# Kernel tuning notes

Measured on AMD Instinct MI355X. Metric: run time of the kernel, lower is better.

The kernel has to match this reference:

```python
import jax, jax.numpy as jnp
import numpy as np

PATCH = 16      # sqrt(n_patches=256)
ALPHA = 10.0
HEADS, DH = 2, 64


def _fourier(coords, Bm):
    # coords: (HW, 2), Bm: (n_features, 2) -> (HW, 2*n_features)
    proj = 2.0 * jnp.pi * coords @ Bm.T
    return jnp.concatenate([jnp.cos(proj), jnp.sin(proj)], axis=-1)


def _forward(coords_decoding, tokens, B_q, B_l0, B_l1,
             qW, qb, toqW, tokvW, tooW, toob,
             bwW0, bwb0, bwW1, bwb1,
             modW0, modb0, modW1, modb1,
             hvW0, hvb0, outW0, outb0, outW1, outb1):
    B = coords_decoding.shape[0]
    Hh, Ww = coords_decoding.shape[1], coords_decoding.shape[2]
    coords = coords_decoding.reshape(B, -1, coords_decoding.shape[-1])
    grid = coords[0]                      # (HW, 2); coords_modulation is None -> same grid
    HW = grid.shape[0]
    m = tokens.shape[1]

    # patch indices and spatial bias
    row = jnp.clip((grid[:, 0] * PATCH).astype(jnp.int32), 0, PATCH - 1)
    col = jnp.clip((grid[:, 1] * PATCH).astype(jnp.int32), 0, PATCH - 1)
    idx = row * PATCH + col               # (HW,)
    t = idx.astype(jnp.float32) / (PATCH * PATCH)
    pos = (jnp.arange(m, dtype=jnp.float32) + 0.5) / m
    rel = -ALPHA * jnp.abs(t[None, :] - pos[:, None]) ** 2   # (m, HW)
    bias = rel.T                          # (HW, m), broadcast over batch & heads

    # query features (shared across batch)
    xq = jax.nn.relu(_fourier(grid, B_q) @ qW + qb)           # (HW, hd)
    xq_b = jnp.broadcast_to(xq[None], (B, HW, xq.shape[-1]))

    # cross attention with spatial bias
    q = (xq_b @ toqW).reshape(B, HW, HEADS, DH).transpose(0, 2, 1, 3)   # (B,h,HW,Dh)
    kv = tokens @ tokvW                                                  # (B,m,2*inner)
    k, v = jnp.split(kv, 2, axis=-1)
    k = k.reshape(B, m, HEADS, DH).transpose(0, 2, 1, 3)                 # (B,h,m,Dh)
    v = v.reshape(B, m, HEADS, DH).transpose(0, 2, 1, 3)
    sim = jnp.einsum('bhqd,bhkd->bhqk', q, k) * (DH ** -0.5) + bias[None, None]
    attn = jax.nn.softmax(sim, axis=-1)
    o = jnp.einsum('bhqk,bhkd->bhqd', attn, v)
    o = o.transpose(0, 2, 1, 3).reshape(B, HW, HEADS * DH)
    mod = o @ tooW + toob                                                # (B,HW,hd)

    # per-band MLP stack (layer_num = 2)
    def band(Bl, bwW, bwb, mW, mb):
        h = jax.nn.relu(_fourier(grid, Bl) @ bwW + bwb)                  # (HW,hd)
        return jax.nn.relu(h[None] + mod @ mW + mb)                      # (B,HW,hd)

    m0 = band(B_l0, bwW0, bwb0, modW0, modb0)
    m1 = band(B_l1, bwW1, bwb1, modW1, modb1)
    hv0 = m0
    hv1 = jax.nn.relu((m1 + hv0) @ hvW0 + hvb0)
    out = (hv0 @ outW0 + outb0) + (hv1 @ outW1 + outb1)                  # (B,HW,3)
    return out.reshape(B, Hh, Ww, -1)


def setup_inputs() -> dict:
    key = jax.random.key(0)
    ks = jax.random.split(key, 32)
    B, H, W, L = 4, 128, 128, 256
    fd, hd, cd, od = 64, 256, 256, 3
    nf = fd // 2
    inner = HEADS * DH

    def lin(k, i, o):
        return jax.random.normal(k, (i, o), dtype=jnp.float32) / np.sqrt(i).astype(np.float32)

    inp = {}
    inp['coords_decoding'] = jax.random.uniform(ks[0], (B, H, W, 2), dtype=jnp.float32)
    inp['tokens'] = jax.random.normal(ks[1], (B, L, cd), dtype=jnp.float32)
    inp['B_q'] = jax.random.normal(ks[2], (nf, 2), dtype=jnp.float32) / 16.0
    inp['B_l0'] = jax.random.normal(ks[3], (nf, 2), dtype=jnp.float32) / 128.0
    inp['B_l1'] = jax.random.normal(ks[4], (nf, 2), dtype=jnp.float32) / 32.0
    inp['qW'] = lin(ks[5], fd, hd); inp['qb'] = jnp.zeros((hd,), jnp.float32)
    inp['toqW'] = lin(ks[6], hd, inner)
    inp['tokvW'] = lin(ks[7], cd, inner * 2)
    inp['tooW'] = lin(ks[8], inner, hd); inp['toob'] = jnp.zeros((hd,), jnp.float32)
    inp['bwW0'] = lin(ks[9], fd, hd); inp['bwb0'] = jnp.zeros((hd,), jnp.float32)
    inp['bwW1'] = lin(ks[10], fd, hd); inp['bwb1'] = jnp.zeros((hd,), jnp.float32)
    inp['modW0'] = lin(ks[11], hd, hd); inp['modb0'] = jnp.zeros((hd,), jnp.float32)
    inp['modW1'] = lin(ks[12], hd, hd); inp['modb1'] = jnp.zeros((hd,), jnp.float32)
    inp['hvW0'] = lin(ks[13], hd, hd); inp['hvb0'] = jnp.zeros((hd,), jnp.float32)
    inp['outW0'] = lin(ks[14], hd, od); inp['outb0'] = jnp.zeros((od,), jnp.float32)
    inp['outW1'] = lin(ks[15], hd, od); inp['outb1'] = jnp.zeros((od,), jnp.float32)
    return inp


def reference(coords_decoding, tokens, B_q, B_l0, B_l1,
              qW, qb, toqW, tokvW, tooW, toob,
              bwW0, bwb0, bwW1, bwb1,
              modW0, modb0, modW1, modb1,
              hvW0, hvb0, outW0, outb0, outW1, outb1):
    return _forward(coords_decoding, tokens, B_q, B_l0, B_l1,
                    qW, qb, toqW, tokvW, tooW, toob,
                    bwW0, bwb0, bwW1, bwb1,
                    modW0, modb0, modW1, modb1,
                    hvW0, hvb0, outW0, outb0, outW1, outb1)
```

## Files before the change

### kernel.cpp

```cpp
#include <hip/hip_runtime.h>
#include <stdint.h>

constexpr int kHW = 16384;
constexpr int kB  = 4;
constexpr int kM  = 256;

typedef _Float16 half8 __attribute__((ext_vector_type(8)));
typedef __attribute__((ext_vector_type(4))) float f32x4;

__device__ __forceinline__ unsigned short f2h(float f) {
  _Float16 h = (_Float16)f;
  return __builtin_bit_cast(unsigned short, h);
}
__device__ __forceinline__ float h2f(unsigned short u) {
  return (float)__builtin_bit_cast(_Float16, u);
}
__device__ __forceinline__ int swz256(int row, int col) {
  int ch = col >> 3;
  ch = (ch & ~7) | ((ch ^ row) & 7);
  return row * 256 + ch * 8 + (col & 7);
}

__global__ __launch_bounds__(256) void wprep_kernel(
    const float* __restrict__ tooW, const float* __restrict__ modW0,
    const float* __restrict__ modW1, const float* __restrict__ hvW0,
    const float* __restrict__ qW, const float* __restrict__ bwW0,
    const float* __restrict__ bwW1, const float* __restrict__ toqW,
    unsigned short* __restrict__ tooWt, unsigned short* __restrict__ modW0t,
    unsigned short* __restrict__ modW1t, unsigned short* __restrict__ hvW0t,
    unsigned short* __restrict__ qWt, unsigned short* __restrict__ bw0t,
    unsigned short* __restrict__ bw1t, unsigned short* __restrict__ toqWt)
{
  int m = blockIdx.x, tid = threadIdx.x;
  const float* Ws[8] = {tooW, modW0, modW1, hvW0, qW, bwW0, bwW1, toqW};
  unsigned short* Wts[8] = {tooWt, modW0t, modW1t, hvW0t, qWt, bw0t, bw1t, toqWt};
  const int Ks[8] = {128, 256, 256, 256, 64, 64, 64, 256};
  const int Ns[8] = {256, 256, 256, 256, 256, 256, 256, 128};
  const float* W = Ws[m];
  unsigned short* Wt = Wts[m];
  int K = Ks[m], N = Ns[m];
  if (tid < N) {
    for (int kb = 0; kb < K / 8; kb++) {
      unsigned short sv[8];
#pragma unroll
      for (int i = 0; i < 8; i++)
        sv[i] = f2h(W[(kb * 8 + i) * N + tid]);
      *(uint4*)&Wt[tid * K + kb * 8] = *(const uint4*)sv;
    }
  }
}

__global__ __launch_bounds__(256) void kv_kernel(
    const float* __restrict__ tokens, const float* __restrict__ tokvW,
    unsigned short* __restrict__ kn_ws, unsigned short* __restrict__ vt_ws)
{
  __shared__ __align__(16) float tok[256];
  int b = blockIdx.y, j = blockIdx.x, c = threadIdx.x;
  tok[c] = tokens[(b * kM + j) * 256 + c];
  __syncthreads();
  float acc = 0.f;
  for (int i4 = 0; i4 < 64; i4++) {
    float4 t4 = *(const float4*)&tok[i4 * 4];
    acc += t4.x * tokvW[(i4*4+0)*256 + c] + t4.y * tokvW[(i4*4+1)*256 + c]
         + t4.z * tokvW[(i4*4+2)*256 + c] + t4.w * tokvW[(i4*4+3)*256 + c];
  }
  unsigned short hv = f2h(acc);
  if (c < 128) {
    int h = c >> 6, dd = c & 63;
    kn_ws[((size_t)(b*2+h)*256 + j) * 64 + dd] = hv;
  } else {
    int c2 = c - 128;
    int h = c2 >> 6, dd = c2 & 63;
    vt_ws[((size_t)(b*2+h)*64 + dd) * 256 + j] = hv;
  }
}

constexpr int kFPitch = 72;
constexpr int kXPitch = 264;

__global__ __launch_bounds__(256, 2) void feat_kernel(
    const float* __restrict__ coords,
    const float* __restrict__ Bq, const float* __restrict__ Bl0, const float* __restrict__ Bl1,
    const float* __restrict__ qb, const float* __restrict__ bwb0, const float* __restrict__ bwb1,
    const unsigned short* __restrict__ qWt, const unsigned short* __restrict__ bw0t,
    const unsigned short* __restrict__ bw1t, const unsigned short* __restrict__ toqWt,
    unsigned short* __restrict__ qc_ws,
    unsigned short* __restrict__ h0_hf, unsigned short* __restrict__ h1_hf)
{
  __shared__ __align__(16) unsigned short ff_s[3][32][kFPitch];
  __shared__ __align__(16) unsigned short xq_s[32][kXPitch];
  __shared__ float coords_s[64];

  int tid = threadIdx.x;
  int px0 = blockIdx.x * 32;
  int w = tid >> 6, ln = tid & 63;
  int c = ln & 15, q = ln >> 4;

  if (tid < 64) coords_s[tid] = coords[px0 * 2 + tid];
  __syncthreads();

#pragma unroll
  for (int r = 0; r < 24; r++) {
    int v = r * 256 + tid;
    int mat = v >> 11;
    int p = (v >> 6) & 31;
    int f = v & 63;
    int fr = f & 31;
    const float* Bm = (mat == 0) ? Bq : (mat == 1 ? Bl0 : Bl1);
    float x = coords_s[p * 2 + 0];
    float y = coords_s[p * 2 + 1];
    float proj = 6.283185307179586f * (x * Bm[fr*2+0] + y * Bm[fr*2+1]);
    float s, cc;
    __sincosf(proj, &s, &cc);
    ff_s[mat][p][f] = f2h((f < 32) ? cc : s);
  }
  __syncthreads();

  const f32x4 zero4 = {0.f, 0.f, 0.f, 0.f};

  for (int mat = 0; mat < 3; mat++) {
    const unsigned short* Wt = (mat == 0) ? qWt : (mat == 1 ? bw0t : bw1t);
    const float* bias = (mat == 0) ? qb : (mat == 1 ? bwb0 : bwb1);
    f32x4 acc[8];
#pragma unroll
    for (int i = 0; i < 8; i++) acc[i] = zero4;
#pragma unroll
    for (int ks = 0; ks < 2; ks++) {
      int koff = ks * 32 + q * 8;
      half8 bfr[4];
#pragma unroll
      for (int nt = 0; nt < 4; nt++)
        bfr[nt] = *(const half8*)(Wt + (size_t)(w*64 + nt*16 + c) * 64 + koff);
      half8 afr[2];
#pragma unroll
      for (int mt = 0; mt < 2; mt++)
        afr[mt] = *(const half8*)(&ff_s[mat][mt*16 + c][koff]);
#pragma unroll
      for (int mt = 0; mt < 2; mt++)
#pragma unroll
        for (int nt = 0; nt < 4; nt++)
          acc[mt*4+nt] = __builtin_amdgcn_mfma_f32_16x16x32_f16(afr[mt], bfr[nt], acc[mt*4+nt], 0, 0, 0);
    }
    float bv[4];
#pragma unroll
    for (int nt = 0; nt < 4; nt++) bv[nt] = bias[w*64 + nt*16 + c];
#pragma unroll
    for (int mt = 0; mt < 2; mt++)
#pragma unroll
      for (int nt = 0; nt < 4; nt++)
#pragma unroll
        for (int rg = 0; rg < 4; rg++) {
          int row = mt*16 + q*4 + rg, col = w*64 + nt*16 + c;
          unsigned short hv = f2h(fmaxf(acc[mt*4+nt][rg] + bv[nt], 0.f));
          if (mat == 0)      xq_s[row][col] = hv;
          else if (mat == 1) h0_hf[((size_t)(px0 + row)) * 256 + col] = hv;
          else               h1_hf[((size_t)(px0 + row)) * 256 + col] = hv;
        }
  }
  __syncthreads();

  {
    f32x4 acc2[4];
#pragma unroll
    for (int i = 0; i < 4; i++) acc2[i] = zero4;
#pragma unroll
    for (int kt = 0; kt < 8; kt++) {
      int koff = kt * 32 + q * 8;
      half8 bfr[2];
#pragma unroll
      for (int nt = 0; nt < 2; nt++)
        bfr[nt] = *(const half8*)(toqWt + (size_t)(w*32 + nt*16 + c) * 256 + koff);
      half8 afr[2];
#pragma unroll
      for (int mt = 0; mt < 2; mt++)
        afr[mt] = *(const half8*)(&xq_s[mt*16 + c][koff]);
#pragma unroll
      for (int mt = 0; mt < 2; mt++)
#pragma unroll
        for (int nt = 0; nt < 2; nt++)
          acc2[mt*2+nt] = __builtin_amdgcn_mfma_f32_16x16x32_f16(afr[mt], bfr[nt], acc2[mt*2+nt], 0, 0, 0);
    }
#pragma unroll
    for (int mt = 0; mt < 2; mt++)
#pragma unroll
      for (int nt = 0; nt < 2; nt++)
#pragma unroll
        for (int rg = 0; rg < 4; rg++) {
          int row = mt*16 + q*4 + rg, col = w*32 + nt*16 + c;
          qc_ws[((size_t)(px0 + row)) * 128 + col] = f2h(acc2[mt*2+nt][rg]);
        }
  }
}

constexpr int kPitch = 264;

template <int KD>
__device__ __forceinline__ void gemm4(
    const unsigned short* abuf, const unsigned short* wt,
    f32x4* acc , int c, int q)
{
#pragma unroll
  for (int ks = 0; ks < KD / 32; ks++) {
    int koff = ks * 32 + q * 8;
    half8 bfr[4];
#pragma unroll
    for (int nt = 0; nt < 4; nt++)
      bfr[nt] = *(const half8*)(wt + (nt * 16 + c) * KD + koff);
    half8 afr[4];
#pragma unroll
    for (int mt = 0; mt < 4; mt++)
      afr[mt] = *(const half8*)(abuf + (mt * 16 + c) * kPitch + koff);
#pragma unroll
    for (int mt = 0; mt < 4; mt++)
#pragma unroll
      for (int nt = 0; nt < 4; nt++)
        acc[mt * 4 + nt] = __builtin_amdgcn_mfma_f32_16x16x32_f16(afr[mt], bfr[nt], acc[mt * 4 + nt], 0, 0, 0);
  }
}

__global__ __launch_bounds__(256, 2) void fused_kernel(
    const unsigned short* __restrict__ kn_ws,
    const unsigned short* __restrict__ vt_ws,
    const unsigned short* __restrict__ qc_ws,
    const float* __restrict__ coords,
    const unsigned short* __restrict__ h0_hf, const unsigned short* __restrict__ h1_hf,
    const unsigned short* __restrict__ tooWt, const float* __restrict__ toob,
    const unsigned short* __restrict__ modW0t, const float* __restrict__ modb0,
    const unsigned short* __restrict__ modW1t, const float* __restrict__ modb1,
    const unsigned short* __restrict__ hvW0t, const float* __restrict__ hvb0,
    const float* __restrict__ outW0, const float* __restrict__ outb0,
    const float* __restrict__ outW1, const float* __restrict__ outb1,
    float* __restrict__ dout)
{
  __shared__ __align__(16) unsigned short buf0[64 * kPitch];
  __shared__ __align__(16) unsigned short regB[64 * kPitch];
  __shared__ __align__(16) unsigned short hbuf[16 * kPitch];
  __shared__ __align__(16) float scratch[64 * 3 * 4];

  unsigned short* buf1  = regB;
  int tid = threadIdx.x;
  int px0 = blockIdx.x * 16;
  int w = tid >> 6, ln = tid & 63;
  int c = ln & 15, q = ln >> 4;
  unsigned short* Pband = regB + w * 4096;

  const f32x4 zero4 = {0.f, 0.f, 0.f, 0.f};

#pragma unroll
  for (int i = 0; i < 2; i++) {
    int idx = i * 256 + tid;
    int p = idx >> 5, c8 = (idx & 31) * 8;
    uint4 v = *(const uint4*)(h0_hf + ((size_t)(px0 + p)) * 256 + c8);
    *(uint4*)&hbuf[p * kPitch + c8] = v;
  }

  float tv[4];
#pragma unroll
  for (int rg = 0; rg < 4; rg++) {
    int px = px0 + q*4 + rg;
    float x = coords[px*2 + 0], y = coords[px*2 + 1];
    int r = min(max((int)(x * 16.0f), 0), 15);
    int cl = min(max((int)(y * 16.0f), 0), 15);
    tv[rg] = (float)(r * 16 + cl) * (1.0f / 256.0f);
  }

  for (int h = 0; h < 2; h++) {
    f32x4 acc[16];
#pragma unroll
    for (int i = 0; i < 16; i++) acc[i] = zero4;
    const unsigned short* kbase = kn_ws + (size_t)(w*2+h) * 256 * 64;
    const unsigned short* qrow = qc_ws + (size_t)(px0 + c) * 128 + h*64;
    half8 a0 = *(const half8*)(qrow + q*8);
    half8 a1 = *(const half8*)(qrow + 32 + q*8);
#pragma unroll
    for (int nt = 0; nt < 16; nt++) {
      const unsigned short* kr = kbase + (size_t)(nt*16 + c) * 64 + q*8;
      half8 b0 = *(const half8*)(kr);
      half8 b1 = *(const half8*)(kr + 32);
      acc[nt] = __builtin_amdgcn_mfma_f32_16x16x32_f16(a0, b0, acc[nt], 0, 0, 0);
      acc[nt] = __builtin_amdgcn_mfma_f32_16x16x32_f16(a1, b1, acc[nt], 0, 0, 0);
    }

    float lm[4];
#pragma unroll
    for (int rg = 0; rg < 4; rg++) {
      float mx = -1e30f;
#pragma unroll
      for (int nt = 0; nt < 16; nt++) {
        float pos = ((float)(nt*16 + c) + 0.5f) * (1.0f / 256.0f);
        float db = tv[rg] - pos;
        float sb = acc[nt][rg] * 0.125f - 10.0f * db * db;
        acc[nt][rg] = sb;
        mx = fmaxf(mx, sb);
      }
      lm[rg] = mx;
    }
#pragma unroll
    for (int s = 1; s < 16; s <<= 1)
#pragma unroll
      for (int rg = 0; rg < 4; rg++)
        lm[rg] = fmaxf(lm[rg], __shfl_xor(lm[rg], s, 64));

    float linv[4];
#pragma unroll
    for (int rg = 0; rg < 4; rg++) {
      float sum = 0.f;
      int row = q*4 + rg;
#pragma unroll
      for (int nt = 0; nt < 16; nt++) {
        float e = __expf(acc[nt][rg] - lm[rg]);
        sum += e;
        Pband[swz256(row, nt*16 + c)] = f2h(e);
      }
      linv[rg] = sum;
    }
#pragma unroll
    for (int s = 1; s < 16; s <<= 1)
#pragma unroll
      for (int rg = 0; rg < 4; rg++)
        linv[rg] += __shfl_xor(linv[rg], s, 64);
#pragma unroll
    for (int rg = 0; rg < 4; rg++) linv[rg] = 1.0f / linv[rg];

    f32x4 oacc[4];
#pragma unroll
    for (int i = 0; i < 4; i++) oacc[i] = zero4;
    const unsigned short* vbase = vt_ws + (size_t)(w*2+h) * 64 * 256;
#pragma unroll
    for (int kt = 0; kt < 8; kt++) {
      int koff = kt * 32 + q * 8;
      half8 af = *(const half8*)&Pband[swz256(c, koff)];
#pragma unroll
      for (int nt = 0; nt < 4; nt++) {
        half8 bf = *(const half8*)(vbase + (size_t)(nt*16 + c) * 256 + koff);
        oacc[nt] = __builtin_amdgcn_mfma_f32_16x16x32_f16(af, bf, oacc[nt], 0, 0, 0);
      }
    }
#pragma unroll
    for (int nt = 0; nt < 4; nt++)
#pragma unroll
      for (int rg = 0; rg < 4; rg++)
        buf0[(w*16 + q*4 + rg) * kPitch + h*64 + nt*16 + c] =
            f2h(oacc[nt][rg] * linv[rg]);
  }
  __syncthreads();

  f32x4 acc[16];

#pragma unroll
  for (int i = 0; i < 16; i++) acc[i] = zero4;
  gemm4<128>(buf0, tooWt + (size_t)w * 64 * 128, acc, c, q);
  {
    float bias[4];
#pragma unroll
    for (int nt = 0; nt < 4; nt++) bias[nt] = toob[w * 64 + nt * 16 + c];
#pragma unroll
    for (int mt = 0; mt < 4; mt++)
#pragma unroll
      for (int nt = 0; nt < 4; nt++)
#pragma unroll
        for (int rg = 0; rg < 4; rg++) {
          int row = mt * 16 + q * 4 + rg, col = w * 64 + nt * 16 + c;
          buf1[row * kPitch + col] = f2h(acc[mt * 4 + nt][rg] + bias[nt]);
        }
  }
  __syncthreads();

#pragma unroll
  for (int i = 0; i < 16; i++) acc[i] = zero4;
  gemm4<256>(buf1, modW0t + (size_t)w * 64 * 256, acc, c, q);
  {
    float bias[4], hr[4][4];
#pragma unroll
    for (int nt = 0; nt < 4; nt++) {
      int col = w * 64 + nt * 16 + c;
      bias[nt] = modb0[col];
#pragma unroll
      for (int rg = 0; rg < 4; rg++)
        hr[nt][rg] = h2f(hbuf[(q * 4 + rg) * kPitch + col]);
    }
#pragma unroll
    for (int mt = 0; mt < 4; mt++)
#pragma unroll
      for (int nt = 0; nt < 4; nt++)
#pragma unroll
        for (int rg = 0; rg < 4; rg++) {
          int row = mt * 16 + q * 4 + rg, col = w * 64 + nt * 16 + c;
          buf0[row * kPitch + col] =
              f2h(fmaxf(acc[mt * 4 + nt][rg] + bias[nt] + hr[nt][rg], 0.f));
        }
  }
  __syncthreads();

#pragma unroll
  for (int i = 0; i < 2; i++) {
    int idx = i * 256 + tid;
    int p = idx >> 5, c8 = (idx & 31) * 8;
    uint4 v = *(const uint4*)(h1_hf + ((size_t)(px0 + p)) * 256 + c8);
    *(uint4*)&hbuf[p * kPitch + c8] = v;
  }
#pragma unroll
  for (int i = 0; i < 16; i++) acc[i] = zero4;
  gemm4<256>(buf1, modW1t + (size_t)w * 64 * 256, acc, c, q);
  __syncthreads();
  {
    float bias[4], hr[4][4];
#pragma unroll
    for (int nt = 0; nt < 4; nt++) {
      int col = w * 64 + nt * 16 + c;
      bias[nt] = modb1[col];
#pragma unroll
      for (int rg = 0; rg < 4; rg++)
        hr[nt][rg] = h2f(hbuf[(q * 4 + rg) * kPitch + col]);
    }
#pragma unroll
    for (int mt = 0; mt < 4; mt++)
#pragma unroll
      for (int nt = 0; nt < 4; nt++)
#pragma unroll
        for (int rg = 0; rg < 4; rg++) {
          int row = mt * 16 + q * 4 + rg, col = w * 64 + nt * 16 + c;
          float m0v = h2f(buf0[row * kPitch + col]);
          float v = m0v + fmaxf(acc[mt * 4 + nt][rg] + bias[nt] + hr[nt][rg], 0.f);
          buf1[row * kPitch + col] = f2h(v);
        }
  }
  __syncthreads();

#pragma unroll
  for (int i = 0; i < 16; i++) acc[i] = zero4;
  gemm4<256>(buf1, hvW0t + (size_t)w * 64 * 256, acc, c, q);
  {
    float bias[4], w0v[4][3], w1v[4][3];
#pragma unroll
    for (int nt = 0; nt < 4; nt++) {
      int col = w * 64 + nt * 16 + c;
      bias[nt] = hvb0[col];
#pragma unroll
      for (int k = 0; k < 3; k++) {
        w0v[nt][k] = outW0[col * 3 + k];
        w1v[nt][k] = outW1[col * 3 + k];
      }
    }
#pragma unroll
    for (int mt = 0; mt < 4; mt++) {
      float pk[4][3];
#pragma unroll
      for (int rg = 0; rg < 4; rg++)
#pragma unroll
        for (int k = 0; k < 3; k++) pk[rg][k] = 0.f;
#pragma unroll
      for (int nt = 0; nt < 4; nt++) {
        int col = w * 64 + nt * 16 + c;
#pragma unroll
        for (int rg = 0; rg < 4; rg++) {
          int row = mt * 16 + q * 4 + rg;
          float hv1 = fmaxf(acc[mt * 4 + nt][rg] + bias[nt], 0.f);
          float m0v = h2f(buf0[row * kPitch + col]);
#pragma unroll
          for (int k = 0; k < 3; k++)
            pk[rg][k] += m0v * w0v[nt][k] + hv1 * w1v[nt][k];
        }
      }
#pragma unroll
      for (int s = 1; s < 16; s <<= 1)
#pragma unroll
        for (int rg = 0; rg < 4; rg++)
#pragma unroll
          for (int k = 0; k < 3; k++)
            pk[rg][k] += __shfl_xor(pk[rg][k], s, 64);
      if (c == 0) {
#pragma unroll
        for (int rg = 0; rg < 4; rg++) {
          int row = mt * 16 + q * 4 + rg;
#pragma unroll
          for (int k = 0; k < 3; k++)
            scratch[row * 12 + k * 4 + w] = pk[rg][k];
        }
      }
    }
  }
  __syncthreads();

  if (tid < 192) {
    int row = tid / 3, k = tid % 3;
    int b = row >> 4, px = px0 + (row & 15);
    float s = outb0[k] + outb1[k];
#pragma unroll
    for (int ww = 0; ww < 4; ww++) s += scratch[row * 12 + k * 4 + ww];
    dout[((size_t)b * kHW + px) * 3 + k] = s;
  }
}

extern "C" void kernel_launch(void* const* d_in, const int* in_sizes, int n_in,
                              void* d_out, int out_size, void* d_ws, size_t ws_size,
                              hipStream_t stream) {
  const float* coords = (const float*)d_in[0];
  const float* tokens = (const float*)d_in[1];
  const float* Bq     = (const float*)d_in[2];
  const float* Bl0    = (const float*)d_in[3];
  const float* Bl1    = (const float*)d_in[4];
  const float* qW     = (const float*)d_in[5];
  const float* qb     = (const float*)d_in[6];
  const float* toqW   = (const float*)d_in[7];
  const float* tokvW  = (const float*)d_in[8];
  const float* tooW   = (const float*)d_in[9];
  const float* toob   = (const float*)d_in[10];
  const float* bwW0   = (const float*)d_in[11];
  const float* bwb0   = (const float*)d_in[12];
  const float* bwW1   = (const float*)d_in[13];
  const float* bwb1   = (const float*)d_in[14];
  const float* modW0  = (const float*)d_in[15];
  const float* modb0  = (const float*)d_in[16];
  const float* modW1  = (const float*)d_in[17];
  const float* modb1  = (const float*)d_in[18];
  const float* hvW0   = (const float*)d_in[19];
  const float* hvb0   = (const float*)d_in[20];
  const float* outW0  = (const float*)d_in[21];
  const float* outb0  = (const float*)d_in[22];
  const float* outW1  = (const float*)d_in[23];
  const float* outb1  = (const float*)d_in[24];

  char* ws = (char*)d_ws;
  unsigned short* qc_ws  = (unsigned short*)(ws + 65536);
  unsigned short* h0_hf  = (unsigned short*)(ws + 4259840);
  unsigned short* h1_hf  = (unsigned short*)(ws + 12648448);
  unsigned short* kn_ws  = (unsigned short*)(ws + 37814272);
  unsigned short* vt_ws  = (unsigned short*)(ws + 38076416);
  unsigned short* tooWt  = (unsigned short*)(ws + 38338560);
  unsigned short* modW0t = (unsigned short*)(ws + 38404096);
  unsigned short* modW1t = (unsigned short*)(ws + 38535168);
  unsigned short* hvW0t  = (unsigned short*)(ws + 38666240);
  unsigned short* qWt    = (unsigned short*)(ws + 38797312);
  unsigned short* bw0t   = (unsigned short*)(ws + 38830080);
  unsigned short* bw1t   = (unsigned short*)(ws + 38862848);
  unsigned short* toqWt  = (unsigned short*)(ws + 38895616);

  wprep_kernel<<<dim3(8), 256, 0, stream>>>(
      tooW, modW0, modW1, hvW0, qW, bwW0, bwW1, toqW,
      tooWt, modW0t, modW1t, hvW0t, qWt, bw0t, bw1t, toqWt);
  feat_kernel<<<dim3(kHW / 32), 256, 0, stream>>>(
      coords, Bq, Bl0, Bl1, qb, bwb0, bwb1,
      qWt, bw0t, bw1t, toqWt,
      qc_ws, h0_hf, h1_hf);
  kv_kernel<<<dim3(kM, kB), 256, 0, stream>>>(tokens, tokvW, kn_ws, vt_ws);
  fused_kernel<<<dim3(kHW / 16), 256, 0, stream>>>(
      kn_ws, vt_ws, qc_ws, coords, h0_hf, h1_hf,
      tooWt, toob, modW0t, modb0, modW1t, modb1,
      hvW0t, hvb0, outW0, outb0, outW1, outb1, (float*)d_out);
}
```

Before: 274.3 us.

## Split fused kernel across batch pairs, drop softmax max pass, swizzle LDS

The fused kernel grid gains a second dimension so each block handles two batches instead of four. Each wave now computes one (batch, head) attention pair, where before it looped over both heads. The softmax max-subtraction pass is removed and exponentials are accumulated directly in two 128-token chunks. LDS buffers shrink to 32 rows with a swizzled layout instead of padded pitch, and launch bounds are raised to 3 blocks per CU. The aim is higher occupancy and fewer serial register-heavy passes. In exchange, per-pixel feature work is duplicated across blocks, and skipping the max subtraction risks overflow if logits grow large.

```diff
diff --git a/kernel.cpp b/kernel.cpp
--- a/kernel.cpp
+++ b/kernel.cpp
@@ -192,33 +192,7 @@
   }
 }
 
-constexpr int kPitch = 264;
-
-template <int KD>
-__device__ __forceinline__ void gemm4(
-    const unsigned short* abuf, const unsigned short* wt,
-    f32x4* acc , int c, int q)
-{
-#pragma unroll
-  for (int ks = 0; ks < KD / 32; ks++) {
-    int koff = ks * 32 + q * 8;
-    half8 bfr[4];
-#pragma unroll
-    for (int nt = 0; nt < 4; nt++)
-      bfr[nt] = *(const half8*)(wt + (nt * 16 + c) * KD + koff);
-    half8 afr[4];
-#pragma unroll
-    for (int mt = 0; mt < 4; mt++)
-      afr[mt] = *(const half8*)(abuf + (mt * 16 + c) * kPitch + koff);
-#pragma unroll
-    for (int mt = 0; mt < 4; mt++)
-#pragma unroll
-      for (int nt = 0; nt < 4; nt++)
-        acc[mt * 4 + nt] = __builtin_amdgcn_mfma_f32_16x16x32_f16(afr[mt], bfr[nt], acc[mt * 4 + nt], 0, 0, 0);
-  }
-}
-
-__global__ __launch_bounds__(256, 2) void fused_kernel(
+__global__ __launch_bounds__(256, 3) void fused_kernel(
     const unsigned short* __restrict__ kn_ws,
     const unsigned short* __restrict__ vt_ws,
     const unsigned short* __restrict__ qc_ws,
@@ -232,17 +206,19 @@
     const float* __restrict__ outW1, const float* __restrict__ outb1,
     float* __restrict__ dout)
 {
-  __shared__ __align__(16) unsigned short buf0[64 * kPitch];
-  __shared__ __align__(16) unsigned short regB[64 * kPitch];
-  __shared__ __align__(16) unsigned short hbuf[16 * kPitch];
-  __shared__ __align__(16) float scratch[64 * 3 * 4];
-
-  unsigned short* buf1  = regB;
+  __shared__ __align__(16) unsigned short buf0[32 * 256];
+  __shared__ __align__(16) unsigned short regB[32 * 256];
+  __shared__ __align__(16) unsigned short hbuf[16 * 264];
+  __shared__ __align__(16) float scratch[32 * 3 * 4];
+
+  unsigned short* buf1 = regB;
   int tid = threadIdx.x;
   int px0 = blockIdx.x * 16;
   int w = tid >> 6, ln = tid & 63;
   int c = ln & 15, q = ln >> 4;
-  unsigned short* Pband = regB + w * 4096;
+  int bl = w >> 1, h = w & 1;
+  int batch = blockIdx.y * 2 + bl;
+  unsigned short* Pband = (w < 2 ? regB : buf0) + (w & 1) * 4096;
 
   const f32x4 zero4 = {0.f, 0.f, 0.f, 0.f};
 
@@ -251,7 +227,7 @@
     int idx = i * 256 + tid;
     int p = idx >> 5, c8 = (idx & 31) * 8;
     uint4 v = *(const uint4*)(h0_hf + ((size_t)(px0 + p)) * 256 + c8);
-    *(uint4*)&hbuf[p * kPitch + c8] = v;
+    *(uint4*)&hbuf[p * 264 + c8] = v;
   }
 
   float tv[4];
@@ -264,111 +240,131 @@
     tv[rg] = (float)(r * 16 + cl) * (1.0f / 256.0f);
   }
 
-  for (int h = 0; h < 2; h++) {
-    f32x4 acc[16];
-#pragma unroll
-    for (int i = 0; i < 16; i++) acc[i] = zero4;
-    const unsigned short* kbase = kn_ws + (size_t)(w*2+h) * 256 * 64;
-    const unsigned short* qrow = qc_ws + (size_t)(px0 + c) * 128 + h*64;
-    half8 a0 = *(const half8*)(qrow + q*8);
-    half8 a1 = *(const half8*)(qrow + 32 + q*8);
-#pragma unroll
-    for (int nt = 0; nt < 16; nt++) {
-      const unsigned short* kr = kbase + (size_t)(nt*16 + c) * 64 + q*8;
+  const unsigned short* qrow = qc_ws + (size_t)(px0 + c) * 128 + h*64;
+  half8 a0 = *(const half8*)(qrow + q*8);
+  half8 a1 = *(const half8*)(qrow + 32 + q*8);
+  const unsigned short* kbase = kn_ws + (size_t)(batch*2+h) * 256 * 64;
+
+  float rsum[4] = {0.f, 0.f, 0.f, 0.f};
+#pragma unroll
+  for (int chunk = 0; chunk < 2; chunk++) {
+    f32x4 acc[8];
+#pragma unroll
+    for (int i = 0; i < 8; i++) acc[i] = zero4;
+#pragma unroll
+    for (int nt = 0; nt < 8; nt++) {
+      const unsigned short* kr = kbase + (size_t)(chunk*128 + nt*16 + c) * 64 + q*8;
       half8 b0 = *(const half8*)(kr);
       half8 b1 = *(const half8*)(kr + 32);
       acc[nt] = __builtin_amdgcn_mfma_f32_16x16x32_f16(a0, b0, acc[nt], 0, 0, 0);
       acc[nt] = __builtin_amdgcn_mfma_f32_16x16x32_f16(a1, b1, acc[nt], 0, 0, 0);
     }
-
-    float lm[4];
 #pragma unroll
     for (int rg = 0; rg < 4; rg++) {
-      float mx = -1e30f;
-#pragma unroll
-      for (int nt = 0; nt < 16; nt++) {
-        float pos = ((float)(nt*16 + c) + 0.5f) * (1.0f / 256.0f);
+#pragma unroll
+      for (int nt = 0; nt < 8; nt++) {
+        int token = chunk*128 + nt*16 + c;
+        float pos = ((float)token + 0.5f) * (1.0f / 256.0f);
         float db = tv[rg] - pos;
-        float sb = acc[nt][rg] * 0.125f - 10.0f * db * db;
-        acc[nt][rg] = sb;
-        mx = fmaxf(mx, sb);
+        float e = __expf(acc[nt][rg] * 0.125f - 10.0f * db * db);
+        rsum[rg] += e;
+        Pband[swz256(q*4 + rg, token)] = f2h(e);
       }
-      lm[rg] = mx;
-    }
-#pragma unroll
-    for (int s = 1; s < 16; s <<= 1)
-#pragma unroll
-      for (int rg = 0; rg < 4; rg++)
-        lm[rg] = fmaxf(lm[rg], __shfl_xor(lm[rg], s, 64));
-
-    float linv[4];
-#pragma unroll
-    for (int rg = 0; rg < 4; rg++) {
-      float sum = 0.f;
-      int row = q*4 + rg;
-#pragma unroll
-      for (int nt = 0; nt < 16; nt++) {
-        float e = __expf(acc[nt][rg] - lm[rg]);
-        sum += e;
-        Pband[swz256(row, nt*16 + c)] = f2h(e);
-      }
-      linv[rg] = sum;
-    }
-#pragma unroll
-    for (int s = 1; s < 16; s <<= 1)
-#pragma unroll
-      for (int rg = 0; rg < 4; rg++)
-        linv[rg] += __shfl_xor(linv[rg], s, 64);
-#pragma unroll
-    for (int rg = 0; rg < 4; rg++) linv[rg] = 1.0f / linv[rg];
-
-    f32x4 oacc[4];
-#pragma unroll
-    for (int i = 0; i < 4; i++) oacc[i] = zero4;
-    const unsigned short* vbase = vt_ws + (size_t)(w*2+h) * 64 * 256;
-#pragma unroll
-    for (int kt = 0; kt < 8; kt++) {
-      int koff = kt * 32 + q * 8;
-      half8 af = *(const half8*)&Pband[swz256(c, koff)];
-#pragma unroll
-      for (int nt = 0; nt < 4; nt++) {
-        half8 bf = *(const half8*)(vbase + (size_t)(nt*16 + c) * 256 + koff);
-        oacc[nt] = __builtin_amdgcn_mfma_f32_16x16x32_f16(af, bf, oacc[nt], 0, 0, 0);
-      }
-    }
+    }
+  }
+#pragma unroll
+  for (int s = 1; s < 16; s <<= 1)
+#pragma unroll
+    for (int rg = 0; rg < 4; rg++)
+      rsum[rg] += __shfl_xor(rsum[rg], s, 64);
+  float linv[4];
+#pragma unroll
+  for (int rg = 0; rg < 4; rg++) linv[rg] = 1.0f / rsum[rg];
+
+  f32x4 oacc[4];
+#pragma unroll
+  for (int i = 0; i < 4; i++) oacc[i] = zero4;
+  const unsigned short* vbase = vt_ws + (size_t)(batch*2+h) * 64 * 256;
+#pragma unroll
+  for (int kt = 0; kt < 8; kt++) {
+    int koff = kt * 32 + q * 8;
+    half8 af = *(const half8*)&Pband[swz256(c, koff)];
+#pragma unroll
+    for (int nt = 0; nt < 4; nt++) {
+      half8 bf = *(const half8*)(vbase + (size_t)(nt*16 + c) * 256 + koff);
+      oacc[nt] = __builtin_amdgcn_mfma_f32_16x16x32_f16(af, bf, oacc[nt], 0, 0, 0);
+    }
+  }
+#pragma unroll
+  for (int nt = 0; nt < 4; nt++)
+#pragma unroll
+    for (int rg = 0; rg < 4; rg++) oacc[nt][rg] *= linv[rg];
+
+  __syncthreads();
+
+#pragma unroll
+  for (int nt = 0; nt < 4; nt++)
+#pragma unroll
+    for (int rg = 0; rg < 4; rg++)
+      buf0[swz256(bl*16 + q*4 + rg, h*64 + nt*16 + c)] = f2h(oacc[nt][rg]);
+  __syncthreads();
+
+  f32x4 acc[8];
+
+#pragma unroll
+  for (int i = 0; i < 8; i++) acc[i] = zero4;
+#pragma unroll
+  for (int ks = 0; ks < 4; ks++) {
+    int koff = ks * 32 + q * 8;
+    half8 bfr[4];
 #pragma unroll
     for (int nt = 0; nt < 4; nt++)
-#pragma unroll
-      for (int rg = 0; rg < 4; rg++)
-        buf0[(w*16 + q*4 + rg) * kPitch + h*64 + nt*16 + c] =
-            f2h(oacc[nt][rg] * linv[rg]);
-  }
-  __syncthreads();
-
-  f32x4 acc[16];
-
-#pragma unroll
-  for (int i = 0; i < 16; i++) acc[i] = zero4;
-  gemm4<128>(buf0, tooWt + (size_t)w * 64 * 128, acc, c, q);
+      bfr[nt] = *(const half8*)(tooWt + (size_t)(w*64 + nt*16 + c) * 128 + koff);
+    half8 afr[2];
+#pragma unroll
+    for (int mt = 0; mt < 2; mt++)
+      afr[mt] = *(const half8*)&buf0[swz256(mt*16 + c, koff)];
+#pragma unroll
+    for (int mt = 0; mt < 2; mt++)
+#pragma unroll
+      for (int nt = 0; nt < 4; nt++)
+        acc[mt*4+nt] = __builtin_amdgcn_mfma_f32_16x16x32_f16(afr[mt], bfr[nt], acc[mt*4+nt], 0, 0, 0);
+  }
+  __syncthreads();
   {
     float bias[4];
 #pragma unroll
     for (int nt = 0; nt < 4; nt++) bias[nt] = toob[w * 64 + nt * 16 + c];
 #pragma unroll
-    for (int mt = 0; mt < 4; mt++)
-#pragma unroll
-      for (int nt = 0; nt < 4; nt++)
-#pragma unroll
-        for (int rg = 0; rg < 4; rg++) {
-          int row = mt * 16 + q * 4 + rg, col = w * 64 + nt * 16 + c;
-          buf1[row * kPitch + col] = f2h(acc[mt * 4 + nt][rg] + bias[nt]);
-        }
-  }
-  __syncthreads();
-
-#pragma unroll
-  for (int i = 0; i < 16; i++) acc[i] = zero4;
-  gemm4<256>(buf1, modW0t + (size_t)w * 64 * 256, acc, c, q);
+    for (int mt = 0; mt < 2; mt++)
+#pragma unroll
+      for (int nt = 0; nt < 4; nt++)
+#pragma unroll
+        for (int rg = 0; rg < 4; rg++)
+          buf1[swz256(mt*16 + q*4 + rg, w*64 + nt*16 + c)] =
+              f2h(acc[mt*4+nt][rg] + bias[nt]);
+  }
+  __syncthreads();
+
+#pragma unroll
+  for (int i = 0; i < 8; i++) acc[i] = zero4;
+#pragma unroll
+  for (int ks = 0; ks < 8; ks++) {
+    int koff = ks * 32 + q * 8;
+    half8 bfr[4];
+#pragma unroll
+    for (int nt = 0; nt < 4; nt++)
+      bfr[nt] = *(const half8*)(modW0t + (size_t)(w*64 + nt*16 + c) * 256 + koff);
+    half8 afr[2];
+#pragma unroll
+    for (int mt = 0; mt < 2; mt++)
+      afr[mt] = *(const half8*)&buf1[swz256(mt*16 + c, koff)];
+#pragma unroll
+    for (int mt = 0; mt < 2; mt++)
+#pragma unroll
+      for (int nt = 0; nt < 4; nt++)
+        acc[mt*4+nt] = __builtin_amdgcn_mfma_f32_16x16x32_f16(afr[mt], bfr[nt], acc[mt*4+nt], 0, 0, 0);
+  }
   {
     float bias[4], hr[4][4];
 #pragma unroll
@@ -377,18 +373,16 @@
       bias[nt] = modb0[col];
 #pragma unroll
       for (int rg = 0; rg < 4; rg++)
-        hr[nt][rg] = h2f(hbuf[(q * 4 + rg) * kPitch + col]);
-    }
-#pragma unroll
-    for (int mt = 0; mt < 4; mt++)
-#pragma unroll
-      for (int nt = 0; nt < 4; nt++)
-#pragma unroll
-        for (int rg = 0; rg < 4; rg++) {
-          int row = mt * 16 + q * 4 + rg, col = w * 64 + nt * 16 + c;
-          buf0[row * kPitch + col] =
-              f2h(fmaxf(acc[mt * 4 + nt][rg] + bias[nt] + hr[nt][rg], 0.f));
-        }
+        hr[nt][rg] = h2f(hbuf[(q * 4 + rg) * 264 + col]);
+    }
+#pragma unroll
+    for (int mt = 0; mt < 2; mt++)
+#pragma unroll
+      for (int nt = 0; nt < 4; nt++)
+#pragma unroll
+        for (int rg = 0; rg < 4; rg++)
+          buf0[swz256(mt*16 + q*4 + rg, w*64 + nt*16 + c)] =
+              f2h(fmaxf(acc[mt*4+nt][rg] + bias[nt] + hr[nt][rg], 0.f));
   }
   __syncthreads();
 
@@ -397,11 +391,27 @@
     int idx = i * 256 + tid;
     int p = idx >> 5, c8 = (idx & 31) * 8;
     uint4 v = *(const uint4*)(h1_hf + ((size_t)(px0 + p)) * 256 + c8);
-    *(uint4*)&hbuf[p * kPitch + c8] = v;
-  }
-#pragma unroll
-  for (int i = 0; i < 16; i++) acc[i] = zero4;
-  gemm4<256>(buf1, modW1t + (size_t)w * 64 * 256, acc, c, q);
+    *(uint4*)&hbuf[p * 264 + c8] = v;
+  }
+#pragma unroll
+  for (int i = 0; i < 8; i++) acc[i] = zero4;
+#pragma unroll
+  for (int ks = 0; ks < 8; ks++) {
+    int koff = ks * 32 + q * 8;
+    half8 bfr[4];
+#pragma unroll
+    for (int nt = 0; nt < 4; nt++)
+      bfr[nt] = *(const half8*)(modW1t + (size_t)(w*64 + nt*16 + c) * 256 + koff);
+    half8 afr[2];
+#pragma unroll
+    for (int mt = 0; mt < 2; mt++)
+      afr[mt] = *(const half8*)&buf1[swz256(mt*16 + c, koff)];
+#pragma unroll
+    for (int mt = 0; mt < 2; mt++)
+#pragma unroll
+      for (int nt = 0; nt < 4; nt++)
+        acc[mt*4+nt] = __builtin_amdgcn_mfma_f32_16x16x32_f16(afr[mt], bfr[nt], acc[mt*4+nt], 0, 0, 0);
+  }
   __syncthreads();
   {
     float bias[4], hr[4][4];
@@ -411,25 +421,41 @@
       bias[nt] = modb1[col];
 #pragma unroll
       for (int rg = 0; rg < 4; rg++)
-        hr[nt][rg] = h2f(hbuf[(q * 4 + rg) * kPitch + col]);
-    }
-#pragma unroll
-    for (int mt = 0; mt < 4; mt++)
+        hr[nt][rg] = h2f(hbuf[(q * 4 + rg) * 264 + col]);
+    }
+#pragma unroll
+    for (int mt = 0; mt < 2; mt++)
 #pragma unroll
       for (int nt = 0; nt < 4; nt++)
 #pragma unroll
         for (int rg = 0; rg < 4; rg++) {
-          int row = mt * 16 + q * 4 + rg, col = w * 64 + nt * 16 + c;
-          float m0v = h2f(buf0[row * kPitch + col]);
-          float v = m0v + fmaxf(acc[mt * 4 + nt][rg] + bias[nt] + hr[nt][rg], 0.f);
-          buf1[row * kPitch + col] = f2h(v);
+          int sidx = swz256(mt*16 + q*4 + rg, w*64 + nt*16 + c);
+          float m0v = h2f(buf0[sidx]);
+          float v = m0v + fmaxf(acc[mt*4+nt][rg] + bias[nt] + hr[nt][rg], 0.f);
+          buf1[sidx] = f2h(v);
         }
   }
   __syncthreads();
 
 #pragma unroll
-  for (int i = 0; i < 16; i++) acc[i] = zero4;
-  gemm4<256>(buf1, hvW0t + (size_t)w * 64 * 256, acc, c, q);
+  for (int i = 0; i < 8; i++) acc[i] = zero4;
+#pragma unroll
+  for (int ks = 0; ks < 8; ks++) {
+    int koff = ks * 32 + q * 8;
+    half8 bfr[4];
+#pragma unroll
+    for (int nt = 0; nt < 4; nt++)
+      bfr[nt] = *(const half8*)(hvW0t + (size_t)(w*64 + nt*16 + c) * 256 + koff);
+    half8 afr[2];
+#pragma unroll
+    for (int mt = 0; mt < 2; mt++)
+      afr[mt] = *(const half8*)&buf1[swz256(mt*16 + c, koff)];
+#pragma unroll
+    for (int mt = 0; mt < 2; mt++)
+#pragma unroll
+      for (int nt = 0; nt < 4; nt++)
+        acc[mt*4+nt] = __builtin_amdgcn_mfma_f32_16x16x32_f16(afr[mt], bfr[nt], acc[mt*4+nt], 0, 0, 0);
+  }
   {
     float bias[4], w0v[4][3], w1v[4][3];
 #pragma unroll
@@ -443,7 +469,7 @@
       }
     }
 #pragma unroll
-    for (int mt = 0; mt < 4; mt++) {
+    for (int mt = 0; mt < 2; mt++) {
       float pk[4][3];
 #pragma unroll
       for (int rg = 0; rg < 4; rg++)
@@ -451,12 +477,10 @@
         for (int k = 0; k < 3; k++) pk[rg][k] = 0.f;
 #pragma unroll
       for (int nt = 0; nt < 4; nt++) {
-        int col = w * 64 + nt * 16 + c;
 #pragma unroll
         for (int rg = 0; rg < 4; rg++) {
-          int row = mt * 16 + q * 4 + rg;
-          float hv1 = fmaxf(acc[mt * 4 + nt][rg] + bias[nt], 0.f);
-          float m0v = h2f(buf0[row * kPitch + col]);
+          float hv1 = fmaxf(acc[mt*4+nt][rg] + bias[nt], 0.f);
+          float m0v = h2f(buf0[swz256(mt*16 + q*4 + rg, w*64 + nt*16 + c)]);
 #pragma unroll
           for (int k = 0; k < 3; k++)
             pk[rg][k] += m0v * w0v[nt][k] + hv1 * w1v[nt][k];
@@ -482,9 +506,9 @@
   }
   __syncthreads();
 
-  if (tid < 192) {
+  if (tid < 96) {
     int row = tid / 3, k = tid % 3;
-    int b = row >> 4, px = px0 + (row & 15);
+    int b = blockIdx.y * 2 + (row >> 4), px = px0 + (row & 15);
     float s = outb0[k] + outb1[k];
 #pragma unroll
     for (int ww = 0; ww < 4; ww++) s += scratch[row * 12 + k * 4 + ww];
@@ -544,7 +568,7 @@
       qWt, bw0t, bw1t, toqWt,
       qc_ws, h0_hf, h1_hf);
   kv_kernel<<<dim3(kM, kB), 256, 0, stream>>>(tokens, tokvW, kn_ws, vt_ws);
-  fused_kernel<<<dim3(kHW / 16), 256, 0, stream>>>(
+  fused_kernel<<<dim3(kHW / 16, 2), 256, 0, stream>>>(
       kn_ws, vt_ws, qc_ws, coords, h0_hf, h1_hf,
       tooWt, toob, modW0t, modb0, modW1t, modb1,
       hvW0t, hvb0, outW0, outb0, outW1, outb1, (float*)d_out);
```

New measurement: 319.7 us. +16.6%, slower.
